# Optimization experiments

Measured on AMD Instinct MI355X. Metric: run time of the kernel, lower is better.

Reference implementation:

```python
import jax, jax.numpy as jnp
import numpy as np

B, T, D, H, L, OUT = 16, 48, 256, 8, 3, 6
STYLE, SKILL = 64, 64


def _ln(x, g, b):
    m = jnp.mean(x, -1, keepdims=True)
    v = jnp.mean((x - m) ** 2, -1, keepdims=True)
    return (x - m) * jax.lax.rsqrt(v + 1e-5) * g + b


def _gelu(x):
    return jax.nn.gelu(x, approximate=False)  # torch 'gelu' activation is exact erf form


def _mha(q_in, kv_in, qkv_w, qkv_b, o_w, o_b, mask):
    d = q_in.shape[-1]
    hd = d // H
    wq, wk, wv = jnp.split(qkv_w, 3, 0)
    bq, bk, bv = jnp.split(qkv_b, 3, 0)

    def heads(x, w, b):
        y = x @ w.T + b
        return y.reshape(y.shape[0], y.shape[1], H, hd)

    q, k, v = heads(q_in, wq, bq), heads(kv_in, wk, bk), heads(kv_in, wv, bv)
    s = jnp.einsum('bqhd,bkhd->bhqk', q, k) / np.float32(np.sqrt(hd))
    if mask is not None:
        s = jnp.where(mask, jnp.float32(-1e9), s)
    a = jax.nn.softmax(s, -1)
    o = jnp.einsum('bhqk,bkhd->bqhd', a, v).reshape(q_in.shape[0], q_in.shape[1], d)
    return o @ o_w.T + o_b


def _pos_encoding():
    pos = jnp.arange(T, dtype=jnp.float32)[:, None]
    div = jnp.exp(jnp.arange(0, D, 2, dtype=jnp.float32) * (-np.log(10000.0) / D))
    pe = jnp.zeros((T, D), jnp.float32)
    pe = pe.at[:, 0::2].set(jnp.sin(pos * div))
    pe = pe.at[:, 1::2].set(jnp.cos(pos * div))
    return pe


def setup_inputs() -> dict:
    key = jax.random.key(0)
    ks = iter(jax.random.split(key, 40))

    def rn(shape, s=0.05):
        return jax.random.normal(next(ks), shape, jnp.float32) * s

    return {
        'z_style': jax.random.normal(next(ks), (B, STYLE), jnp.float32),
        'z_skill': jax.random.normal(next(ks), (B, SKILL), jnp.float32),
        'start_token': jnp.zeros((1, 1, OUT), jnp.float32),
        'mem_w1': rn((D, STYLE + SKILL)), 'mem_b1': jnp.zeros((D,), jnp.float32),
        'mem_ln_g': jnp.ones((D,), jnp.float32), 'mem_ln_b': jnp.zeros((D,), jnp.float32),
        'mem_w2': rn((D, D)), 'mem_b2': jnp.zeros((D,), jnp.float32),
        'emb_w': rn((D, OUT)), 'emb_b': jnp.zeros((D,), jnp.float32),
        'sa_qkv_w': rn((L, 3 * D, D)), 'sa_qkv_b': jnp.zeros((L, 3 * D), jnp.float32),
        'sa_o_w': rn((L, D, D)), 'sa_o_b': jnp.zeros((L, D), jnp.float32),
        'ca_qkv_w': rn((L, 3 * D, D)), 'ca_qkv_b': jnp.zeros((L, 3 * D), jnp.float32),
        'ca_o_w': rn((L, D, D)), 'ca_o_b': jnp.zeros((L, D), jnp.float32),
        'ln1_g': jnp.ones((L, D), jnp.float32), 'ln1_b': jnp.zeros((L, D), jnp.float32),
        'ln2_g': jnp.ones((L, D), jnp.float32), 'ln2_b': jnp.zeros((L, D), jnp.float32),
        'ln3_g': jnp.ones((L, D), jnp.float32), 'ln3_b': jnp.zeros((L, D), jnp.float32),
        'ff1_w': rn((L, 4 * D, D)), 'ff1_b': jnp.zeros((L, 4 * D), jnp.float32),
        'ff2_w': rn((L, D, 4 * D)), 'ff2_b': jnp.zeros((L, D), jnp.float32),
        'op_w1': rn((D // 2, D)), 'op_b1': jnp.zeros((D // 2,), jnp.float32),
        'op_w2': rn((OUT, D // 2)), 'op_b2': jnp.zeros((OUT,), jnp.float32),
    }


def reference(z_style, z_skill, start_token, mem_w1, mem_b1, mem_ln_g, mem_ln_b,
              mem_w2, mem_b2, emb_w, emb_b, sa_qkv_w, sa_qkv_b, sa_o_w, sa_o_b,
              ca_qkv_w, ca_qkv_b, ca_o_w, ca_o_b, ln1_g, ln1_b, ln2_g, ln2_b,
              ln3_g, ln3_b, ff1_w, ff1_b, ff2_w, ff2_b, op_w1, op_b1, op_w2, op_b2):
    # memory: [B,1,D] expanded to seq_len (identical rows, as in the torch module)
    cond = jnp.concatenate([z_style, z_skill], -1)
    h = _gelu(_ln(cond @ mem_w1.T + mem_b1, mem_ln_g, mem_ln_b))
    memory = jnp.broadcast_to((h @ mem_w2.T + mem_b2)[:, None, :], (B, T, D))

    pe = _pos_encoding()
    causal = jnp.triu(jnp.ones((T, T), bool), 1)  # True = masked (future)
    layer_ps = (sa_qkv_w, sa_qkv_b, sa_o_w, sa_o_b, ca_qkv_w, ca_qkv_b, ca_o_w,
                ca_o_b, ln1_g, ln1_b, ln2_g, ln2_b, ln3_g, ln3_b,
                ff1_w, ff1_b, ff2_w, ff2_b)

    def layer_step(x, p):
        (sqw, sqb, sow, sob, cqw, cqb, cow, cob, g1, b1, g2, b2, g3, b3,
         f1w, f1b, f2w, f2b) = p
        # post-norm TransformerDecoderLayer (torch default norm_first=False)
        x = _ln(x + _mha(x, x, sqw, sqb, sow, sob, causal), g1, b1)
        x = _ln(x + _mha(x, memory, cqw, cqb, cow, cob, None), g2, b2)
        x = _ln(x + (_gelu(x @ f1w.T + f1b) @ f2w.T + f2b), g3, b3)
        return x, None

    def t_step(inputs, t):
        # Causal mask => decoded[:, t] depends only on inputs[:, :t+1]; running the
        # padded full-length decoder reproduces the torch growing-prefix loop exactly.
        x = inputs @ emb_w.T + emb_b + pe[None]
        dec, _ = jax.lax.scan(layer_step, x, layer_ps)
        d_t = jax.lax.dynamic_slice(dec, (0, t, 0), (B, 1, D))[:, 0]
        out_t = _gelu(d_t @ op_w1.T + op_b1) @ op_w2.T + op_b2
        inputs = jax.lax.dynamic_update_slice(inputs, out_t[:, None, :], (0, t + 1, 0))
        return inputs, out_t

    inputs0 = jnp.zeros((B, T, OUT), jnp.float32).at[:, 0:1, :].set(
        jnp.broadcast_to(start_token, (B, 1, OUT)))
    _, ys = jax.lax.scan(t_step, inputs0, jnp.arange(T))
    return jnp.transpose(ys, (1, 0, 2))  # [B, T, OUT]
```

## Files before the change

### kernel.cpp

```cpp
#include <hip/hip_runtime.h>
#include <hip/hip_bf16.h>
#include <math.h>

#define NGRP 16
#define GWG  8
#define NBLK (NGRP*GWG)
#define NTHR 512
#define TSEQ 48
#define DDIM 256
#define HDIM 32
#define NLAY 3
#define NOUT 6

#define CNT_OFF   0u
#define CNT_BYTES 16384u
#define GRP_OFF   16384u
#define GRP_STRF  5120u
#define PO_F   0
#define PF_F   2048
#define CAL_F  4096
#define WB_OFF 360448u
#define WOFF_QKV 0u
#define WOFF_WO  589824u
#define WOFF_F1  786432u
#define WOFF_F2  1572864u
#define WOFF_OP1 2359296u
#define NCVT     2392064u

typedef __attribute__((address_space(1))) const unsigned int gu32;
typedef __attribute__((address_space(3))) unsigned int lu32;

__device__ __forceinline__ void gl_lds16(const unsigned short* g, unsigned short* l) {
  __builtin_amdgcn_global_load_lds((gu32*)g, (lu32*)l, 16, 0, 0);
}
__device__ __forceinline__ void bfp(unsigned int u, float& lo, float& hi) {
  union { unsigned int i; float f; } a, b;
  a.i = u << 16; b.i = u & 0xffff0000u; lo = a.f; hi = b.f;
}
__device__ __forceinline__ float gelu_exact(float x) {
  return 0.5f * x * (1.0f + erff(x * 0.70710678118654752f));
}
__device__ __forceinline__ float dot8(const uint4& u, const float* x, int k0) {
  float lo, hi, acc = 0.f;
  bfp(u.x, lo, hi); acc += x[k0  ]*lo + x[k0+1]*hi;
  bfp(u.y, lo, hi); acc += x[k0+2]*lo + x[k0+3]*hi;
  bfp(u.z, lo, hi); acc += x[k0+4]*lo + x[k0+5]*hi;
  bfp(u.w, lo, hi); acc += x[k0+6]*lo + x[k0+7]*hi;
  return acc;
}

__global__ void convert_bf16(const float* qkv, const float* ow, const float* f1,
                             const float* f2, const float* w1, unsigned char* ws) {
  __hip_bfloat16* dst = (__hip_bfloat16*)(ws + WB_OFF);
  size_t stride = (size_t)gridDim.x * blockDim.x;
  for (size_t i = (size_t)blockIdx.x * blockDim.x + threadIdx.x; i < NCVT; i += stride) {
    float v;
    if      (i < WOFF_WO)  v = qkv[i];
    else if (i < WOFF_F1)  v = ow[i - WOFF_WO];
    else if (i < WOFF_F2)  v = f1[i - WOFF_F1];
    else if (i < WOFF_OP1) v = f2[i - WOFF_F2];
    else                   v = w1[i - WOFF_OP1];
    dst[i] = __float2bfloat16(v);
  }
}

__global__ void precompute_ca(const float* zs, const float* zk,
                              const float* mw1, const float* mb1,
                              const float* mlg, const float* mlb,
                              const float* mw2, const float* mb2,
                              const float* cqw, const float* cqb,
                              const float* cow, const float* cob,
                              unsigned char* ws) {
  const int g = blockIdx.x & 15, l = blockIdx.x >> 4;
  const int tid = threadIdx.x;
  __shared__ float cond[128], h[256], mvv[256], vv[256], lred[16];

  auto lnstat = [&](float v, float& m, float& rs) {
    float a = v, b = v * v;
    #pragma unroll
    for (int off = 32; off; off >>= 1) { a += __shfl_xor(a, off); b += __shfl_xor(b, off); }
    if ((tid & 63) == 0) { lred[tid >> 6] = a; lred[4 + (tid >> 6)] = b; }
    __syncthreads();
    float sa = lred[0]+lred[1]+lred[2]+lred[3];
    float sb = lred[4]+lred[5]+lred[6]+lred[7];
    m = sa * (1.0f/256.0f);
    rs = rsqrtf(sb * (1.0f/256.0f) - m*m + 1e-5f);
    __syncthreads();
  };

  if (tid < 128) cond[tid] = (tid < 64) ? zs[g*64 + tid] : zk[g*64 + tid - 64];
  __syncthreads();
  float acc = mb1[tid];
  { const float* w = mw1 + (size_t)tid * 128;
    for (int k = 0; k < 128; k += 4) {
      float4 q = *(const float4*)(w + k);
      acc += q.x*cond[k] + q.y*cond[k+1] + q.z*cond[k+2] + q.w*cond[k+3];
    } }
  float m, rs; lnstat(acc, m, rs);
  h[tid] = gelu_exact((acc - m) * rs * mlg[tid] + mlb[tid]);
  __syncthreads();
  float a2 = mb2[tid];
  { const float* w = mw2 + (size_t)tid * 256;
    for (int k = 0; k < 256; k += 4) {
      float4 q = *(const float4*)(w + k);
      a2 += q.x*h[k] + q.y*h[k+1] + q.z*h[k+2] + q.w*h[k+3];
    } }
  mvv[tid] = a2;
  __syncthreads();
  float a3 = cqb[l*768 + 512 + tid];
  { const float* w = cqw + ((size_t)l*768 + 512 + tid) * 256;
    for (int k = 0; k < 256; k += 4) {
      float4 q = *(const float4*)(w + k);
      a3 += q.x*mvv[k] + q.y*mvv[k+1] + q.z*mvv[k+2] + q.w*mvv[k+3];
    } }
  vv[tid] = a3;
  __syncthreads();
  float a4 = cob[l*256 + tid];
  { const float* w = cow + ((size_t)l*256 + tid) * 256;
    for (int k = 0; k < 256; k += 4) {
      float4 q = *(const float4*)(w + k);
      a4 += q.x*vv[k] + q.y*vv[k+1] + q.z*vv[k+2] + q.w*vv[k+3];
    } }
  ((float*)(ws + GRP_OFF))[(size_t)g * GRP_STRF + CAL_F + l*256 + tid] = a4;
}

struct DecP {
  const float *start_token, *emb_w, *emb_b;
  const float *sa_qkv_b, *sa_o_b;
  const float *ln1_g, *ln1_b, *ln2_g, *ln2_b, *ln3_g, *ln3_b;
  const float *ff1_b, *ff2_b;
  const float *op_b1, *op_w2, *op_b2;
  float* out;
  unsigned char* ws;
};

__global__ __launch_bounds__(NTHR, 1) void decoder_persistent(DecP p) {
  const int g = blockIdx.x % NGRP;
  const int s = blockIdx.x / NGRP;
  const int tid = threadIdx.x;

  unsigned int* flg = (unsigned int*)(p.ws + CNT_OFF) + (size_t)g * 256;
  float* grp = (float*)(p.ws + GRP_OFF) + (size_t)g * GRP_STRF;
  float* Po = grp + PO_F;
  float* Pf = grp + PF_F;
  const float* CALW = grp + CAL_F;
  const unsigned short* WB = (const unsigned short*)(p.ws + WB_OFF);

  __shared__ __align__(16) unsigned short Rws[32768];
  __shared__ float xls[DDIM], x2ls[DDIM], red[NTHR], lred[32], fxl[128];
  __shared__ float qb[HDIM], ah[HDIM], sc[64];
  __shared__ float kc[NLAY*TSEQ*33], vc[NLAY*TSEQ*33];
  __shared__ float cals[768], obias[768], ff2b[768];
  __shared__ float ln1g[768], ln1b[768], ln2g[768], ln2b[768], ln3g[768], ln3b[768];
  __shared__ float qkvb[288], ff1b[384];
  __shared__ float embw[DDIM*NOUT], embb[DDIM];
  __shared__ float opb1[128], opw2[NOUT*128], opb2[8], OUTV[8];

  const int row = tid >> 2, kk = tid & 3;
  const int oB = tid & 255, khB = tid >> 8;
  const int wv = tid >> 6, ln = tid & 63;

  auto stage_qkv = [&](int l) {
    #pragma unroll
    for (int r = 0; r < 6; ++r) {
      int c = (r*8 + wv)*64 + ln;
      int rw = c >> 5, wc = (c & 31) ^ (rw & 7);
      const unsigned short* gp = WB + WOFF_QKV
        + ((size_t)(l*768 + (rw>>5)*256 + s*32 + (rw&31)))*256 + wc*8;
      gl_lds16(gp, Rws + (size_t)(r*8 + wv)*512);
    }
  };
  auto stage_ff1 = [&](int l) {
    #pragma unroll
    for (int r = 0; r < 8; ++r) {
      int c = (r*8 + wv)*64 + ln;
      int rw = c >> 5, wc = (c & 31) ^ (rw & 7);
      const unsigned short* gp = WB + WOFF_F1
        + ((size_t)(l*1024 + s*128 + rw))*256 + wc*8;
      gl_lds16(gp, Rws + (size_t)(r*8 + wv)*512);
    }
  };
  auto stage_ff2 = [&](int l) {
    #pragma unroll
    for (int r = 0; r < 8; ++r) {
      int c = (r*8 + wv)*64 + ln;
      int rw = c >> 4, wc = (c & 15) ^ (rw & 15);
      const unsigned short* gp = WB + WOFF_F2
        + ((size_t)(l*256 + rw))*1024 + s*128 + wc*8;
      gl_lds16(gp, Rws + (size_t)(r*8 + wv)*512);
    }
  };

  uint4 pWO[2], pO1[8];
  auto ldWO = [&](int l) {
    const unsigned short* w = WB + WOFF_WO + ((size_t)(l*256 + oB))*256 + s*32 + khB*16;
    pWO[0] = *(const uint4*)(w);
    pWO[1] = *(const uint4*)(w + 8);
  };
  auto ldO1 = [&]() {
    const unsigned short* w = WB + WOFF_OP1 + (size_t)row*256 + kk*64;
    #pragma unroll
    for (int i = 0; i < 8; ++i) pO1[i] = *(const uint4*)(w + i*8);
  };

  unsigned int barcount = 0;
  auto gbar = [&]() {
    __syncthreads();
    ++barcount;
    if (tid == 0)
      __hip_atomic_store(flg + s*32, barcount, __ATOMIC_RELEASE, __HIP_MEMORY_SCOPE_AGENT);
    if (tid < GWG) {
      while (__hip_atomic_load(flg + tid*32, __ATOMIC_RELAXED, __HIP_MEMORY_SCOPE_AGENT) < barcount) {}
    }
    if (tid == 0)
      (void)__hip_atomic_load(flg + s*32, __ATOMIC_ACQUIRE, __HIP_MEMORY_SCOPE_AGENT);
    __syncthreads();
  };

  auto lnstats = [&](float v, float* slot, float& m, float& rs) {
    float a = v, b = v * v;
    #pragma unroll
    for (int off = 32; off; off >>= 1) { a += __shfl_xor(a, off); b += __shfl_xor(b, off); }
    if ((tid & 63) == 0 && tid < 256) { slot[tid >> 6] = a; slot[4 + (tid >> 6)] = b; }
    __syncthreads();
    float sa = slot[0]+slot[1]+slot[2]+slot[3];
    float sb = slot[4]+slot[5]+slot[6]+slot[7];
    m = sa * (1.0f/256.0f);
    rs = rsqrtf(sb * (1.0f/256.0f) - m*m + 1e-5f);
  };

  for (int i = tid; i < 768; i += NTHR) {
    cals[i]  = CALW[i];
    obias[i] = p.sa_o_b[i];
    ff2b[i]  = p.ff2_b[i];
    ln1g[i] = p.ln1_g[i]; ln1b[i] = p.ln1_b[i];
    ln2g[i] = p.ln2_g[i]; ln2b[i] = p.ln2_b[i];
    ln3g[i] = p.ln3_g[i]; ln3b[i] = p.ln3_b[i];
  }
  for (int i = tid; i < 288; i += NTHR) {
    int l = i / 96, r = i % 96, sect = (r >> 5), o = r & 31;
    qkvb[i] = p.sa_qkv_b[l*768 + sect*256 + s*32 + o];
  }
  for (int i = tid; i < 384; i += NTHR) {
    int l = i >> 7, o = i & 127;
    ff1b[i] = p.ff1_b[l*1024 + s*128 + o];
  }
  for (int i = tid; i < DDIM*NOUT; i += NTHR) embw[i] = p.emb_w[i];
  for (int i = tid; i < DDIM; i += NTHR) embb[i] = p.emb_b[i];
  for (int i = tid; i < 128; i += NTHR) opb1[i] = p.op_b1[i];
  for (int i = tid; i < NOUT*128; i += NTHR) opw2[i] = p.op_w2[i];
  if (tid < NOUT) OUTV[tid] = p.start_token[tid];
  if (tid < 8) opb2[tid] = (tid < NOUT) ? p.op_b2[tid] : 0.f;

  const float divv = (tid < 256) ? expf(-0.035977892078031968f * (float)(2*(tid>>1))) : 0.f;
  __syncthreads();

  if (tid < 256) {
    float acc = embb[tid] + ((tid & 1) ? 1.0f : 0.0f);
    #pragma unroll
    for (int j = 0; j < NOUT; ++j) acc += OUTV[j] * embw[tid*NOUT + j];
    xls[tid] = acc;
  }
  stage_qkv(0);
  ldWO(0);
  __syncthreads();

  for (int t = 0; t < TSEQ; ++t) {
    for (int l = 0; l < NLAY; ++l) {
      if (l > 0) {
        float r2 = 0.f;
        if (tid < 256) {
          r2 = x2ls[tid] + ff2b[(l-1)*256 + tid];
          #pragma unroll
          for (int ss = 0; ss < GWG; ++ss) r2 += Pf[ss*256 + tid];
        }
        float m, rs; lnstats(r2, lred + 0, m, rs);
        if (tid < 256)
          xls[tid] = (r2 - m) * rs * ln3g[(l-1)*256 + tid] + ln3b[(l-1)*256 + tid];
        __syncthreads();
      }
      if (row < 96) {
        float acc = 0.f;
        #pragma unroll
        for (int i = 0; i < 8; ++i) {
          int ii = (i + kk) & 7;
          int k0 = kk*64 + ii*8;
          const uint4 w = *(const uint4*)(Rws + row*256 + (k0 ^ ((row&7)<<3)));
          acc += dot8(w, xls, k0);
        }
        acc += __shfl_xor(acc, 1);
        acc += __shfl_xor(acc, 2);
        if (kk == 0) {
          float v = acc + qkvb[l*96 + row];
          int sect = row >> 5, o = row & 31;
          if (sect == 0) qb[o] = v;
          else if (sect == 1) kc[(l*TSEQ + t)*33 + o] = v;
          else vc[(l*TSEQ + t)*33 + o] = v;
        }
      }
      __syncthreads();
      stage_ff1(l);
      if (tid < 64) {
        float scj = -1e30f;
        if (tid <= t) {
          const float* kr = &kc[(l*TSEQ + tid)*33];
          float a = 0.f;
          #pragma unroll
          for (int d = 0; d < HDIM; ++d) a += qb[d] * kr[d];
          scj = a * 0.17677669529663687f;
        }
        float mx = scj;
        #pragma unroll
        for (int off = 32; off; off >>= 1) mx = fmaxf(mx, __shfl_xor(mx, off));
        float e = (tid <= t) ? expf(scj - mx) : 0.f;
        float su = e;
        #pragma unroll
        for (int off = 32; off; off >>= 1) su += __shfl_xor(su, off);
        sc[tid] = e / su;
      }
      __syncthreads();
      if (tid < 256) {
        int d = tid >> 3, jg = tid & 7;
        float acc = 0.f;
        for (int j = jg; j <= t; j += 8) acc += sc[j] * vc[(l*TSEQ + j)*33 + d];
        acc += __shfl_xor(acc, 1);
        acc += __shfl_xor(acc, 2);
        acc += __shfl_xor(acc, 4);
        if (jg == 0) ah[d] = acc;
      }
      __syncthreads();
      red[tid] = dot8(pWO[0], ah, khB*16) + dot8(pWO[1], ah, khB*16 + 8);
      __syncthreads();
      if (tid < 256) Po[s*256 + tid] = red[tid] + red[tid + 256];
      gbar();

      float r = 0.f;
      if (tid < 256) {
        r = xls[tid] + obias[l*256 + tid];
        #pragma unroll
        for (int ss = 0; ss < GWG; ++ss) r += Po[ss*256 + tid];
      }
      float m1, rs1; lnstats(r, lred + 8, m1, rs1);
      float z = 0.f;
      if (tid < 256)
        z = (r - m1)*rs1*ln1g[l*256 + tid] + ln1b[l*256 + tid] + cals[l*256 + tid];
      float m2, rs2; lnstats(z, lred + 16, m2, rs2);
      if (tid < 256) x2ls[tid] = (z - m2)*rs2*ln2g[l*256 + tid] + ln2b[l*256 + tid];
      __syncthreads();
      float facc = 0.f;
      {
        #pragma unroll
        for (int i = 0; i < 8; ++i) {
          int ii = (i + kk) & 7;
          int k0 = kk*64 + ii*8;
          const uint4 w = *(const uint4*)(Rws + row*256 + (k0 ^ ((row&7)<<3)));
          facc += dot8(w, x2ls, k0);
        }
        facc += __shfl_xor(facc, 1);
        facc += __shfl_xor(facc, 2);
      }
      __syncthreads();
      stage_ff2(l);
      if (kk == 0) fxl[row] = gelu_exact(facc + ff1b[l*128 + row]);
      __syncthreads();
      {
        float acc = 0.f;
        #pragma unroll
        for (int j = 0; j < 8; ++j) {
          int k0 = khB*64 + j*8;
          const uint4 w = *(const uint4*)(Rws + oB*128 + (k0 ^ ((oB&15)<<3)));
          acc += dot8(w, fxl, k0);
        }
        red[tid] = acc;
      }
      __syncthreads();
      {
        int lnx = (l == 2) ? 0 : l + 1;
        stage_qkv(lnx);
        ldWO(lnx);
        if (l == 2) ldO1();
      }
      if (tid < 256) Pf[s*256 + tid] = red[tid] + red[tid + 256];
      gbar();
    }

    {
      float r2 = 0.f;
      if (tid < 256) {
        r2 = x2ls[tid] + ff2b[2*256 + tid];
        #pragma unroll
        for (int ss = 0; ss < GWG; ++ss) r2 += Pf[ss*256 + tid];
      }
      float m, rs; lnstats(r2, lred + 24, m, rs);
      if (tid < 256) xls[tid] = (r2 - m)*rs*ln3g[2*256 + tid] + ln3b[2*256 + tid];
      __syncthreads();
      float oacc = 0.f;
      #pragma unroll
      for (int i = 0; i < 8; ++i) oacc += dot8(pO1[i], xls, kk*64 + i*8);
      oacc += __shfl_xor(oacc, 1);
      oacc += __shfl_xor(oacc, 2);
      if (kk == 0) fxl[row] = gelu_exact(oacc + opb1[row]);
      __syncthreads();
      if (tid < 192) {
        int oo = tid >> 5, kl = tid & 31;
        float acc = fxl[kl]*opw2[oo*128 + kl] + fxl[kl+32]*opw2[oo*128 + kl+32]
                  + fxl[kl+64]*opw2[oo*128 + kl+64] + fxl[kl+96]*opw2[oo*128 + kl+96];
        #pragma unroll
        for (int off = 16; off; off >>= 1) acc += __shfl_xor(acc, off);
        if (kl == 0) {
          float v = acc + opb2[oo];
          OUTV[oo] = v;
          if (s == 0) p.out[((size_t)g*TSEQ + t)*NOUT + oo] = v;
        }
      }
      __syncthreads();
      if (tid < 256) {
        float ang = (float)(t + 1) * divv;
        float pe = (tid & 1) ? cosf(ang) : sinf(ang);
        float acc = embb[tid] + pe;
        #pragma unroll
        for (int j = 0; j < NOUT; ++j) acc += OUTV[j] * embw[tid*NOUT + j];
        xls[tid] = acc;
      }
      __syncthreads();
    }
  }
}

extern "C" void kernel_launch(void* const* d_in, const int* in_sizes, int n_in,
                              void* d_out, int out_size, void* d_ws, size_t ws_size,
                              hipStream_t stream) {
  const float* const* F = (const float* const*)d_in;
  const float* z_style = F[0]; const float* z_skill = F[1];
  DecP p;
  p.start_token = F[2];
  const float* mem_w1 = F[3]; const float* mem_b1 = F[4];
  const float* mem_ln_g = F[5]; const float* mem_ln_b = F[6];
  const float* mem_w2 = F[7]; const float* mem_b2 = F[8];
  p.emb_w = F[9]; p.emb_b = F[10];
  const float* sa_qkv_w = F[11]; p.sa_qkv_b = F[12];
  const float* sa_o_w  = F[13]; p.sa_o_b = F[14];
  const float* ca_qkv_w = F[15]; const float* ca_qkv_b = F[16];
  const float* ca_o_w = F[17]; const float* ca_o_b = F[18];
  p.ln1_g = F[19]; p.ln1_b = F[20]; p.ln2_g = F[21]; p.ln2_b = F[22];
  p.ln3_g = F[23]; p.ln3_b = F[24];
  const float* ff1_w = F[25]; p.ff1_b = F[26];
  const float* ff2_w = F[27]; p.ff2_b = F[28];
  const float* op_w1 = F[29]; p.op_b1 = F[30]; p.op_w2 = F[31]; p.op_b2 = F[32];
  p.out = (float*)d_out;
  p.ws  = (unsigned char*)d_ws;

  hipMemsetAsync((char*)d_ws + CNT_OFF, 0, CNT_BYTES, stream);
  convert_bf16<<<dim3(512), dim3(256), 0, stream>>>(sa_qkv_w, sa_o_w, ff1_w, ff2_w, op_w1,
                                                    (unsigned char*)d_ws);
  precompute_ca<<<dim3(48), dim3(256), 0, stream>>>(z_style, z_skill, mem_w1, mem_b1,
                                                    mem_ln_g, mem_ln_b, mem_w2, mem_b2,
                                                    ca_qkv_w, ca_qkv_b, ca_o_w, ca_o_b,
                                                    (unsigned char*)d_ws);
  decoder_persistent<<<dim3(NBLK), dim3(NTHR), 0, stream>>>(p);
}
```

Baseline: 2.036 ms.

## Remap block-to-group ids and drop split-K reduction in WO/FF2 partial GEMVs

Block-to-group mapping changes so that the 8 workgroups of a group are consecutive block ids rather than strided. That can change placement and locality for the per-group barrier spinning. The WO and FF2 partial GEMVs now use 256 threads, each computing a full dot product. This removes the shared-memory split-K reduction and one __syncthreads, at the cost of leaving half the threads idle and giving each active thread a longer serial dot.

```diff
diff --git a/kernel.cpp b/kernel.cpp
--- a/kernel.cpp
+++ b/kernel.cpp
@@ -135,8 +135,8 @@
 };
 
 __global__ __launch_bounds__(NTHR, 1) void decoder_persistent(DecP p) {
-  const int g = blockIdx.x % NGRP;
-  const int s = blockIdx.x / NGRP;
+  const int g = blockIdx.x >> 3;
+  const int s = blockIdx.x & 7;
   const int tid = threadIdx.x;
 
   unsigned int* flg = (unsigned int*)(p.ws + CNT_OFF) + (size_t)g * 256;
@@ -157,7 +157,6 @@
   __shared__ float opb1[128], opw2[NOUT*128], opb2[8], OUTV[8];
 
   const int row = tid >> 2, kk = tid & 3;
-  const int oB = tid & 255, khB = tid >> 8;
   const int wv = tid >> 6, ln = tid & 63;
 
   auto stage_qkv = [&](int l) {
@@ -191,11 +190,13 @@
     }
   };
 
-  uint4 pWO[2], pO1[8];
+  uint4 pWO[4], pO1[8];
   auto ldWO = [&](int l) {
-    const unsigned short* w = WB + WOFF_WO + ((size_t)(l*256 + oB))*256 + s*32 + khB*16;
-    pWO[0] = *(const uint4*)(w);
-    pWO[1] = *(const uint4*)(w + 8);
+    if (tid < 256) {
+      const unsigned short* w = WB + WOFF_WO + ((size_t)(l*256 + tid))*256 + s*32;
+      #pragma unroll
+      for (int c = 0; c < 4; ++c) pWO[c] = *(const uint4*)(w + c*8);
+    }
   };
   auto ldO1 = [&]() {
     const unsigned short* w = WB + WOFF_OP1 + (size_t)row*256 + kk*64;
@@ -329,9 +330,12 @@
         if (jg == 0) ah[d] = acc;
       }
       __syncthreads();
-      red[tid] = dot8(pWO[0], ah, khB*16) + dot8(pWO[1], ah, khB*16 + 8);
-      __syncthreads();
-      if (tid < 256) Po[s*256 + tid] = red[tid] + red[tid + 256];
+      if (tid < 256) {
+        float acc = 0.f;
+        #pragma unroll
+        for (int c = 0; c < 4; ++c) acc += dot8(pWO[c], ah, c*8);
+        Po[s*256 + tid] = acc;
+      }
       gbar();
 
       float r = 0.f;
@@ -363,15 +367,15 @@
       stage_ff2(l);
       if (kk == 0) fxl[row] = gelu_exact(facc + ff1b[l*128 + row]);
       __syncthreads();
-      {
-        float acc = 0.f;
-        #pragma unroll
-        for (int j = 0; j < 8; ++j) {
-          int k0 = khB*64 + j*8;
-          const uint4 w = *(const uint4*)(Rws + oB*128 + (k0 ^ ((oB&15)<<3)));
-          acc += dot8(w, fxl, k0);
-        }
-        red[tid] = acc;
+      if (tid < 256) {
+        float acc2 = 0.f;
+        #pragma unroll
+        for (int j2 = 0; j2 < 16; ++j2) {
+          int k0 = j2*8;
+          const uint4 w = *(const uint4*)(Rws + tid*128 + (k0 ^ ((tid&15)<<3)));
+          acc2 += dot8(w, fxl, k0);
+        }
+        Pf[s*256 + tid] = acc2;
       }
       __syncthreads();
       {
@@ -380,7 +384,6 @@
         ldWO(lnx);
         if (l == 2) ldO1();
       }
-      if (tid < 256) Pf[s*256 + tid] = red[tid] + red[tid + 256];
       gbar();
     }
 
```

Measured after the change: 2.334 ms. 14.6% more time.
